# Kernel optimization log

Hardware: AMD Instinct MI355X
Metric: run time of the kernel (lower is better)

## Reference

```python
import jax, jax.numpy as jnp
import numpy as np

N = 50000
D_IN = 1024          # BioGPT hidden size
HID = 256            # gnn_hidden_dim
H1, H2 = 4, 1        # heads per layer
NEG_SLOPE = 0.2      # PyG GATv2 default


def _glorot(key, shape):
    fan_in, fan_out = shape[0], shape[-1]
    lim = (6.0 / (fan_in + fan_out)) ** 0.5
    return jax.random.uniform(key, shape, jnp.float32, -lim, lim)


def setup_inputs() -> dict:
    key = jax.random.key(0)
    ks = jax.random.split(key, 12)
    node_features = jax.random.normal(ks[0], (N, D_IN), jnp.float32)
    edge_index = jax.random.randint(ks[1], (2, 400000), 0, N, jnp.int64)
    return {
        "node_features": node_features,
        "edge_index": edge_index,
        # layer 1: GATv2Conv(1024 -> 256, heads=4)
        "W1_l": _glorot(ks[2], (D_IN, H1 * HID)),
        "b1_l": jnp.zeros((H1 * HID,), jnp.float32),
        "W1_r": _glorot(ks[3], (D_IN, H1 * HID)),
        "b1_r": jnp.zeros((H1 * HID,), jnp.float32),
        "att1": _glorot(ks[4], (H1, HID)),
        "bias1": jnp.zeros((H1 * HID,), jnp.float32),
        # layer 2: GATv2Conv(1024 -> 256, heads=1)
        "W2_l": _glorot(ks[5], (H1 * HID, H2 * HID)),
        "b2_l": jnp.zeros((H2 * HID,), jnp.float32),
        "W2_r": _glorot(ks[6], (H1 * HID, H2 * HID)),
        "b2_r": jnp.zeros((H2 * HID,), jnp.float32),
        "att2": _glorot(ks[7], (H2, HID)),
        "bias2": jnp.zeros((H2 * HID,), jnp.float32),
    }


def _gatv2(x, src, dst, Wl, bl, Wr, br, att, bias, heads):
    n = x.shape[0]
    xl = (x @ Wl + bl).reshape(n, heads, HID)  # source-side transform
    xr = (x @ Wr + br).reshape(n, heads, HID)  # target-side transform
    msg = xl[src] + xr[dst]                    # [E, H, C]
    e = jnp.where(msg > 0, msg, NEG_SLOPE * msg)
    alpha = jnp.einsum('ehc,hc->eh', e, att)   # attention logits
    amax = jax.ops.segment_max(alpha, dst, num_segments=n)
    ex = jnp.exp(alpha - amax[dst])
    denom = jax.ops.segment_sum(ex, dst, num_segments=n)
    a = ex / (denom[dst] + 1e-16)              # segment softmax per dst node
    out = jax.ops.segment_sum(a[:, :, None] * xl[src], dst, num_segments=n)
    return out.reshape(n, heads * HID) + bias


def reference(node_features, edge_index, W1_l, b1_l, W1_r, b1_r, att1, bias1,
              W2_l, b2_l, W2_r, b2_r, att2, bias2):
    n = node_features.shape[0]
    loops = jnp.arange(n, dtype=edge_index.dtype)
    src = jnp.concatenate([edge_index[0], loops])  # add self-loops (PyG default)
    dst = jnp.concatenate([edge_index[1], loops])
    x = _gatv2(node_features, src, dst, W1_l, b1_l, W1_r, b1_r, att1, bias1, H1)
    x = jax.nn.relu(x)
    # dropout(p=0.1) is identity in eval mode
    x = _gatv2(x, src, dst, W2_l, b2_l, W2_r, b2_r, att2, bias2, H2)
    return jax.nn.relu(x)
```

## Files before the change

kernel.cpp:

```cpp
#include <hip/hip_runtime.h>
#include <stdint.h>

#define D_IN 1024
#define C1   1024
#define C2   256
#define NEG  0.2f

typedef unsigned int u32;
typedef uint16_t u16;
typedef __attribute__((ext_vector_type(8))) short bf16x8;
typedef __attribute__((ext_vector_type(4))) float f32x4;

__device__ __forceinline__ float bf2f(u32 lo16) { return __uint_as_float(lo16 << 16); }
__device__ __forceinline__ u16 f2bf(float f) {
  u32 u = __float_as_uint(f);
  u += 0x7fffu + ((u >> 16) & 1u);
  return (u16)(u >> 16);
}

__device__ __forceinline__ void gload16(const u16* g, u16* l) {
  __builtin_amdgcn_global_load_lds(
      (const __attribute__((address_space(1))) unsigned int*)g,
      (__attribute__((address_space(3))) unsigned int*)l,
      16, 0, 0);
}

__global__ void cast_x_k(const float* __restrict__ x, u16* __restrict__ A,
                         int nrows, int Mp) {
  long long idx = (long long)blockIdx.x * blockDim.x + threadIdx.x;
  long long total = (long long)Mp * (D_IN / 8);
  if (idx >= total) return;
  long long base = idx * 8;
  int row = (int)(base >> 10);
  u32 o0 = 0, o1 = 0, o2 = 0, o3 = 0;
  if (row < nrows) {
    const float4* px = (const float4*)(x + base);
    float4 v0 = px[0], v1 = px[1];
    o0 = (u32)f2bf(v0.x) | ((u32)f2bf(v0.y) << 16);
    o1 = (u32)f2bf(v0.z) | ((u32)f2bf(v0.w) << 16);
    o2 = (u32)f2bf(v1.x) | ((u32)f2bf(v1.y) << 16);
    o3 = (u32)f2bf(v1.z) | ((u32)f2bf(v1.w) << 16);
  }
  *(uint4*)(A + base) = make_uint4(o0, o1, o2, o3);
}

__global__ void transpose_cast_k(const float* __restrict__ W, u16* __restrict__ Wt,
                                 int K, int Nc) {
  __shared__ float sh[32][33];
  int k0 = blockIdx.x * 32, n0 = blockIdx.y * 32;
  int tx = threadIdx.x, ty = threadIdx.y;
#pragma unroll
  for (int i = 0; i < 32; i += 8)
    sh[ty + i][tx] = W[(long long)(k0 + ty + i) * Nc + (n0 + tx)];
  __syncthreads();
#pragma unroll
  for (int i = 0; i < 32; i += 8)
    Wt[(long long)(n0 + ty + i) * K + (k0 + tx)] = f2bf(sh[tx][ty + i]);
}

__global__ void concat_bias_k(const float* __restrict__ a, const float* __restrict__ b,
                              float* __restrict__ o, int na, int nb) {
  int i = blockIdx.x * 256 + threadIdx.x;
  if (i < na) o[i] = a[i];
  else if (i < na + nb) o[i] = b[i - na];
}

template <int TN>
__global__ __launch_bounds__(512, 2) void gemm8_k(
    const u16* __restrict__ A, const u16* __restrict__ Bt,
    const float* __restrict__ bias, u16* __restrict__ C, int K) {
  __shared__ u16 As[2][2][8192];
  __shared__ u16 Bs[2][2][8192];
  const int nx = gridDim.x, ny = gridDim.y;
  const int nwg = nx * ny;
  int id = blockIdx.y * nx + blockIdx.x;
  int q = nwg >> 3, r = nwg & 7;
  int xcd = id & 7, loc = id >> 3;
  int sid = (xcd < r ? xcd * (q + 1) : r * (q + 1) + (xcd - r) * q) + loc;
  const int m0 = (sid / ny) * 256;
  const int n0 = (sid % ny) * 256;

  const int tid = threadIdx.x;
  const int lane = tid & 63;
  const int wave = tid >> 6;
  const int wm = wave >> 2;
  const int wn = wave & 3;
  const int bh = wn >> 1;
  const int bql = (wn & 1) * 2048;

  const int srow = tid >> 2;
  const int kq   = tid & 3;
  const int ksw  = (kq ^ ((srow >> 1) & 3)) * 8;

  const int nt = K / 64;

  const u16* gA[2] = { A + (long long)(m0 + srow) * K + ksw,
                       A + (long long)(m0 + 128 + srow) * K + ksw };
  const u16* gB[2] = { Bt + (long long)(n0 + srow) * K + ksw,
                       Bt + (long long)(n0 + 128 + srow) * K + ksw };

  auto stageA = [&](int kt, int h) {
    int db = kt & 1;
    gload16(gA[h] + kt * 64,      &As[db][h][tid * 8]);
    gload16(gA[h] + kt * 64 + 32, &As[db][h][4096 + tid * 8]);
  };
  auto stageB = [&](int kt, int h) {
    int db = kt & 1;
    gload16(gB[h] + kt * 64,      &Bs[db][h][tid * 8]);
    gload16(gB[h] + kt * 64 + 32, &Bs[db][h][4096 + tid * 8]);
  };

  const int rbase = (lane & 15) * 32 + (((lane >> 4) ^ ((lane >> 1) & 3)) << 3);

  f32x4 acc[8][4] = {};
  bf16x8 av[4][2], bv[4][2];

  stageA(0, 0); stageA(0, 1); stageB(0, 0); stageB(0, 1);
  if (nt > 1) {
    stageB(1, 0); stageB(1, 1);
    asm volatile("s_waitcnt vmcnt(4)" ::: "memory");
  } else {
    asm volatile("s_waitcnt vmcnt(0)" ::: "memory");
  }
  __builtin_amdgcn_s_barrier();

  for (int t = 0; t < nt; ++t) {
    const int cur = t & 1;
    const u16* Al = &As[cur][wm][0];
    const u16* Bl = &Bs[cur][bh][0];

    if (t + 1 < nt) stageA(t + 1, 0);
#pragma unroll
    for (int i = 0; i < 4; ++i) {
      av[i][0] = *(const bf16x8*)(Al + i * 512 + rbase);
      av[i][1] = *(const bf16x8*)(Al + 4096 + i * 512 + rbase);
    }
#pragma unroll
    for (int j = 0; j < 2; ++j) {
      bv[j][0] = *(const bf16x8*)(Bl + bql + j * 512 + rbase);
      bv[j][1] = *(const bf16x8*)(Bl + 4096 + bql + j * 512 + rbase);
    }
    __builtin_amdgcn_s_barrier();
    __builtin_amdgcn_s_setprio(1);
#pragma unroll
    for (int i = 0; i < 4; ++i)
#pragma unroll
      for (int j = 0; j < 2; ++j) {
        acc[i][j] = __builtin_amdgcn_mfma_f32_16x16x32_bf16(av[i][0], bv[j][0], acc[i][j], 0, 0, 0);
        acc[i][j] = __builtin_amdgcn_mfma_f32_16x16x32_bf16(av[i][1], bv[j][1], acc[i][j], 0, 0, 0);
      }
    __builtin_amdgcn_s_setprio(0);
    __builtin_amdgcn_s_barrier();

    if (t + 1 < nt) stageA(t + 1, 1);
#pragma unroll
    for (int j = 2; j < 4; ++j) {
      bv[j][0] = *(const bf16x8*)(Bl + bql + j * 512 + rbase);
      bv[j][1] = *(const bf16x8*)(Bl + 4096 + bql + j * 512 + rbase);
    }
    __builtin_amdgcn_s_barrier();
    __builtin_amdgcn_s_setprio(1);
#pragma unroll
    for (int i = 0; i < 4; ++i)
#pragma unroll
      for (int j = 2; j < 4; ++j) {
        acc[i][j] = __builtin_amdgcn_mfma_f32_16x16x32_bf16(av[i][0], bv[j][0], acc[i][j], 0, 0, 0);
        acc[i][j] = __builtin_amdgcn_mfma_f32_16x16x32_bf16(av[i][1], bv[j][1], acc[i][j], 0, 0, 0);
      }
    __builtin_amdgcn_s_setprio(0);
    __builtin_amdgcn_s_barrier();

    if (t + 2 < nt) stageB(t + 2, 0);
#pragma unroll
    for (int i = 0; i < 4; ++i) {
      av[i][0] = *(const bf16x8*)(Al + (4 + i) * 512 + rbase);
      av[i][1] = *(const bf16x8*)(Al + 4096 + (4 + i) * 512 + rbase);
    }
    __builtin_amdgcn_s_barrier();
    __builtin_amdgcn_s_setprio(1);
#pragma unroll
    for (int i = 0; i < 4; ++i)
#pragma unroll
      for (int j = 2; j < 4; ++j) {
        acc[4 + i][j] = __builtin_amdgcn_mfma_f32_16x16x32_bf16(av[i][0], bv[j][0], acc[4 + i][j], 0, 0, 0);
        acc[4 + i][j] = __builtin_amdgcn_mfma_f32_16x16x32_bf16(av[i][1], bv[j][1], acc[4 + i][j], 0, 0, 0);
      }
    __builtin_amdgcn_s_setprio(0);
    __builtin_amdgcn_s_barrier();

    if (t + 2 < nt) stageB(t + 2, 1);
    __builtin_amdgcn_s_barrier();
    __builtin_amdgcn_s_setprio(1);
#pragma unroll
    for (int i = 0; i < 4; ++i)
#pragma unroll
      for (int j = 0; j < 2; ++j) {
        acc[4 + i][j] = __builtin_amdgcn_mfma_f32_16x16x32_bf16(av[i][0], bv[j][0], acc[4 + i][j], 0, 0, 0);
        acc[4 + i][j] = __builtin_amdgcn_mfma_f32_16x16x32_bf16(av[i][1], bv[j][1], acc[4 + i][j], 0, 0, 0);
      }
    __builtin_amdgcn_s_setprio(0);
    if (t + 2 < nt) {
      asm volatile("s_waitcnt vmcnt(4)" ::: "memory");
    } else if (t + 1 < nt) {
      asm volatile("s_waitcnt vmcnt(0)" ::: "memory");
    }
    __builtin_amdgcn_s_barrier();
  }

#pragma unroll
  for (int mf = 0; mf < 8; ++mf) {
    int r0 = m0 + wm * 128 + mf * 16 + ((lane >> 4) << 2);
#pragma unroll
    for (int nf = 0; nf < 4; ++nf) {
      int c = n0 + wn * 64 + nf * 16 + (lane & 15);
      float b = bias[c];
#pragma unroll
      for (int j = 0; j < 4; ++j)
        C[(long long)(r0 + j) * TN + c] = f2bf(acc[mf][nf][j] + b);
    }
  }
}

__global__ void count_k(const int* __restrict__ ei, int* __restrict__ counts,
                        int E0, int E) {
  for (int e = blockIdx.x * blockDim.x + threadIdx.x; e < E;
       e += gridDim.x * blockDim.x) {
    int dst = (e < E0) ? ei[E0 + e] : e - E0;
    atomicAdd(&counts[dst], 1);
  }
}

__global__ void blocksum_k(const int* __restrict__ counts, int* __restrict__ bsum, int n) {
  int i = blockIdx.x * 256 + threadIdx.x;
  int v = (i < n) ? counts[i] : 0;
#pragma unroll
  for (int off = 1; off < 64; off <<= 1) v += __shfl_xor(v, off);
  __shared__ int sh[4];
  if ((threadIdx.x & 63) == 0) sh[threadIdx.x >> 6] = v;
  __syncthreads();
  if (threadIdx.x == 0) bsum[blockIdx.x] = sh[0] + sh[1] + sh[2] + sh[3];
}

__global__ void scanb_k(const int* __restrict__ bsum, int* __restrict__ boff,
                        int nb, int* __restrict__ indptr, int n, int E) {
  __shared__ int sh[256];
  int i = threadIdx.x;
  int v = (i < nb) ? bsum[i] : 0;
  sh[i] = v;
  __syncthreads();
  int sum = v;
  for (int off = 1; off < 256; off <<= 1) {
    int t = (i >= off) ? sh[i - off] : 0;
    __syncthreads();
    sum += t;
    sh[i] = sum;
    __syncthreads();
  }
  if (i < nb) boff[i] = sum - v;
  if (i == 0) indptr[n] = E;
}

__global__ void scanf_k(const int* __restrict__ counts, const int* __restrict__ boff,
                        int* __restrict__ indptr, int n) {
  __shared__ int sh[256];
  int b = blockIdx.x;
  int i = b * 256 + threadIdx.x;
  int v = (i < n) ? counts[i] : 0;
  sh[threadIdx.x] = v;
  __syncthreads();
  int sum = v;
  for (int off = 1; off < 256; off <<= 1) {
    int t = (threadIdx.x >= off) ? sh[threadIdx.x - off] : 0;
    __syncthreads();
    sum += t;
    sh[threadIdx.x] = sum;
    __syncthreads();
  }
  if (i < n) indptr[i] = boff[b] + sum - v;
}

__global__ void scatter_k(const int* __restrict__ ei, const int* __restrict__ indptr,
                          int* __restrict__ cursor, int* __restrict__ esrc,
                          int E0, int E) {
  for (int e = blockIdx.x * blockDim.x + threadIdx.x; e < E;
       e += gridDim.x * blockDim.x) {
    int dst, src;
    if (e < E0) { src = ei[e]; dst = ei[E0 + e]; } else { src = dst = e - E0; }
    int pos = atomicAdd(&cursor[dst], 1);
    esrc[indptr[dst] + pos] = src;
  }
}

__global__ __launch_bounds__(256) void fused_edge1_k(
    const u16* __restrict__ XLR, const int* __restrict__ indptr,
    const int* __restrict__ esrc, const float* __restrict__ att,
    const float* __restrict__ bias, u16* __restrict__ X2, int N) {
  int d = blockIdx.x;
  int tid = threadIdx.x;
  int c0 = tid * 4;
  if (d >= N) {
    *(ushort4*)(X2 + (long long)d * C1 + c0) = make_ushort4(0, 0, 0, 0);
    return;
  }
  ushort4 xr4 = *(const ushort4*)(XLR + (long long)d * 2048 + 1024 + c0);
  float xr0 = bf2f(xr4.x), xr1 = bf2f(xr4.y), xr2 = bf2f(xr4.z), xr3 = bf2f(xr4.w);
  float4 at = *(const float4*)(att + c0);

  float m = -INFINITY, l = 0.f;
  float a0 = 0.f, a1 = 0.f, a2 = 0.f, a3 = 0.f;
  int p = indptr[d], pend = indptr[d + 1];
  ushort4 z4 = make_ushort4(0, 0, 0, 0);
#define LD1(ix) (*(const ushort4*)(XLR + (long long)esrc[ix] * 2048 + c0))
  ushort4 qa = (p < pend) ? LD1(p) : z4;
  ushort4 qb = (p + 1 < pend) ? LD1(p + 1) : z4;
  ushort4 ra = (p + 2 < pend) ? LD1(p + 2) : z4;
  ushort4 rb = (p + 3 < pend) ? LD1(p + 3) : z4;
  int i = p;
  for (; i + 1 < pend; i += 2) {
    ushort4 ca = qa, cb = qb;
    qa = ra; qb = rb;
    ra = (i + 4 < pend) ? LD1(i + 4) : z4;
    rb = (i + 5 < pend) ? LD1(i + 5) : z4;
    float xa0 = bf2f(ca.x), xa1 = bf2f(ca.y), xa2 = bf2f(ca.z), xa3 = bf2f(ca.w);
    float xb0 = bf2f(cb.x), xb1 = bf2f(cb.y), xb2 = bf2f(cb.z), xb3 = bf2f(cb.w);
    float ta0 = xa0 + xr0, ta1 = xa1 + xr1, ta2 = xa2 + xr2, ta3 = xa3 + xr3;
    float tb0 = xb0 + xr0, tb1 = xb1 + xr1, tb2 = xb2 + xr2, tb3 = xb3 + xr3;
    ta0 = ta0 > 0.f ? ta0 : NEG * ta0;  ta1 = ta1 > 0.f ? ta1 : NEG * ta1;
    ta2 = ta2 > 0.f ? ta2 : NEG * ta2;  ta3 = ta3 > 0.f ? ta3 : NEG * ta3;
    tb0 = tb0 > 0.f ? tb0 : NEG * tb0;  tb1 = tb1 > 0.f ? tb1 : NEG * tb1;
    tb2 = tb2 > 0.f ? tb2 : NEG * tb2;  tb3 = tb3 > 0.f ? tb3 : NEG * tb3;
    float sa = at.x * ta0 + at.y * ta1 + at.z * ta2 + at.w * ta3;
    float sb = at.x * tb0 + at.y * tb1 + at.z * tb2 + at.w * tb3;
#pragma unroll
    for (int off = 1; off < 64; off <<= 1) {
      sa += __shfl_xor(sa, off);
      sb += __shfl_xor(sb, off);
    }
    float mnew = fmaxf(fmaxf(m, sa), sb);
    float scale = __expf(m - mnew);
    float wa = __expf(sa - mnew);
    float wb = __expf(sb - mnew);
    l = l * scale + wa + wb;
    a0 = a0 * scale + wa * xa0 + wb * xb0;
    a1 = a1 * scale + wa * xa1 + wb * xb1;
    a2 = a2 * scale + wa * xa2 + wb * xb2;
    a3 = a3 * scale + wa * xa3 + wb * xb3;
    m = mnew;
  }
  if (i < pend) {
    float xa0 = bf2f(qa.x), xa1 = bf2f(qa.y), xa2 = bf2f(qa.z), xa3 = bf2f(qa.w);
    float ta0 = xa0 + xr0, ta1 = xa1 + xr1, ta2 = xa2 + xr2, ta3 = xa3 + xr3;
    ta0 = ta0 > 0.f ? ta0 : NEG * ta0;  ta1 = ta1 > 0.f ? ta1 : NEG * ta1;
    ta2 = ta2 > 0.f ? ta2 : NEG * ta2;  ta3 = ta3 > 0.f ? ta3 : NEG * ta3;
    float sa = at.x * ta0 + at.y * ta1 + at.z * ta2 + at.w * ta3;
#pragma unroll
    for (int off = 1; off < 64; off <<= 1) sa += __shfl_xor(sa, off);
    float mnew = fmaxf(m, sa);
    float scale = __expf(m - mnew);
    float wa = __expf(sa - mnew);
    l = l * scale + wa;
    a0 = a0 * scale + wa * xa0;
    a1 = a1 * scale + wa * xa1;
    a2 = a2 * scale + wa * xa2;
    a3 = a3 * scale + wa * xa3;
  }
#undef LD1
  float inv = 1.f / (l + 1e-16f);
  float4 b = *(const float4*)(bias + c0);
  ushort4 o;
  o.x = f2bf(fmaxf(a0 * inv + b.x, 0.f));
  o.y = f2bf(fmaxf(a1 * inv + b.y, 0.f));
  o.z = f2bf(fmaxf(a2 * inv + b.z, 0.f));
  o.w = f2bf(fmaxf(a3 * inv + b.w, 0.f));
  *(ushort4*)(X2 + (long long)d * C1 + c0) = o;
}

__global__ __launch_bounds__(256) void fused_edge2_k(
    const u16* __restrict__ XLR, const int* __restrict__ indptr,
    const int* __restrict__ esrc, const float* __restrict__ att,
    const float* __restrict__ bias, float* __restrict__ out, int N) {
  int d = blockIdx.x * 4 + (threadIdx.x >> 6);
  if (d >= N) return;
  int lane = threadIdx.x & 63;
  int c0 = lane * 4;
  ushort4 xr4 = *(const ushort4*)(XLR + (long long)d * 512 + 256 + c0);
  float xr0 = bf2f(xr4.x), xr1 = bf2f(xr4.y), xr2 = bf2f(xr4.z), xr3 = bf2f(xr4.w);
  float4 at = *(const float4*)(att + c0);

  float m = -INFINITY, l = 0.f;
  float a0 = 0.f, a1 = 0.f, a2 = 0.f, a3 = 0.f;
  int p = indptr[d], pend = indptr[d + 1];
  ushort4 z4 = make_ushort4(0, 0, 0, 0);
#define LD2(ix) (*(const ushort4*)(XLR + (long long)esrc[ix] * 512 + c0))
  ushort4 qa = (p < pend) ? LD2(p) : z4;
  ushort4 qb = (p + 1 < pend) ? LD2(p + 1) : z4;
  ushort4 ra = (p + 2 < pend) ? LD2(p + 2) : z4;
  ushort4 rb = (p + 3 < pend) ? LD2(p + 3) : z4;
  int i = p;
  for (; i + 1 < pend; i += 2) {
    ushort4 ca = qa, cb = qb;
    qa = ra; qb = rb;
    ra = (i + 4 < pend) ? LD2(i + 4) : z4;
    rb = (i + 5 < pend) ? LD2(i + 5) : z4;
    float xa0 = bf2f(ca.x), xa1 = bf2f(ca.y), xa2 = bf2f(ca.z), xa3 = bf2f(ca.w);
    float xb0 = bf2f(cb.x), xb1 = bf2f(cb.y), xb2 = bf2f(cb.z), xb3 = bf2f(cb.w);
    float ta0 = xa0 + xr0, ta1 = xa1 + xr1, ta2 = xa2 + xr2, ta3 = xa3 + xr3;
    float tb0 = xb0 + xr0, tb1 = xb1 + xr1, tb2 = xb2 + xr2, tb3 = xb3 + xr3;
    ta0 = ta0 > 0.f ? ta0 : NEG * ta0;  ta1 = ta1 > 0.f ? ta1 : NEG * ta1;
    ta2 = ta2 > 0.f ? ta2 : NEG * ta2;  ta3 = ta3 > 0.f ? ta3 : NEG * ta3;
    tb0 = tb0 > 0.f ? tb0 : NEG * tb0;  tb1 = tb1 > 0.f ? tb1 : NEG * tb1;
    tb2 = tb2 > 0.f ? tb2 : NEG * tb2;  tb3 = tb3 > 0.f ? tb3 : NEG * tb3;
    float sa = at.x * ta0 + at.y * ta1 + at.z * ta2 + at.w * ta3;
    float sb = at.x * tb0 + at.y * tb1 + at.z * tb2 + at.w * tb3;
#pragma unroll
    for (int off = 1; off < 64; off <<= 1) {
      sa += __shfl_xor(sa, off);
      sb += __shfl_xor(sb, off);
    }
    float mnew = fmaxf(fmaxf(m, sa), sb);
    float scale = __expf(m - mnew);
    float wa = __expf(sa - mnew);
    float wb = __expf(sb - mnew);
    l = l * scale + wa + wb;
    a0 = a0 * scale + wa * xa0 + wb * xb0;
    a1 = a1 * scale + wa * xa1 + wb * xb1;
    a2 = a2 * scale + wa * xa2 + wb * xb2;
    a3 = a3 * scale + wa * xa3 + wb * xb3;
    m = mnew;
  }
  if (i < pend) {
    float xa0 = bf2f(qa.x), xa1 = bf2f(qa.y), xa2 = bf2f(qa.z), xa3 = bf2f(qa.w);
    float ta0 = xa0 + xr0, ta1 = xa1 + xr1, ta2 = xa2 + xr2, ta3 = xa3 + xr3;
    ta0 = ta0 > 0.f ? ta0 : NEG * ta0;  ta1 = ta1 > 0.f ? ta1 : NEG * ta1;
    ta2 = ta2 > 0.f ? ta2 : NEG * ta2;  ta3 = ta3 > 0.f ? ta3 : NEG * ta3;
    float sa = at.x * ta0 + at.y * ta1 + at.z * ta2 + at.w * ta3;
#pragma unroll
    for (int off = 1; off < 64; off <<= 1) sa += __shfl_xor(sa, off);
    float mnew = fmaxf(m, sa);
    float scale = __expf(m - mnew);
    float wa = __expf(sa - mnew);
    l = l * scale + wa;
    a0 = a0 * scale + wa * xa0;
    a1 = a1 * scale + wa * xa1;
    a2 = a2 * scale + wa * xa2;
    a3 = a3 * scale + wa * xa3;
  }
#undef LD2
  float inv = 1.f / (l + 1e-16f);
  float4 b = *(const float4*)(bias + c0);
  float4 o;
  o.x = fmaxf(a0 * inv + b.x, 0.f);
  o.y = fmaxf(a1 * inv + b.y, 0.f);
  o.z = fmaxf(a2 * inv + b.z, 0.f);
  o.w = fmaxf(a3 * inv + b.w, 0.f);
  *(float4*)(out + (long long)d * C2 + c0) = o;
}

extern "C" void kernel_launch(void* const* d_in, const int* in_sizes, int n_in,
                              void* d_out, int out_size, void* d_ws, size_t ws_size,
                              hipStream_t stream) {
  const float* x     = (const float*)d_in[0];
  const int*   ei    = (const int*)d_in[1];
  const float* W1l   = (const float*)d_in[2];
  const float* b1l   = (const float*)d_in[3];
  const float* W1r   = (const float*)d_in[4];
  const float* b1r   = (const float*)d_in[5];
  const float* att1  = (const float*)d_in[6];
  const float* bias1 = (const float*)d_in[7];
  const float* W2l   = (const float*)d_in[8];
  const float* b2l   = (const float*)d_in[9];
  const float* W2r   = (const float*)d_in[10];
  const float* b2r   = (const float*)d_in[11];
  const float* att2  = (const float*)d_in[12];
  const float* bias2 = (const float*)d_in[13];

  const int N  = in_sizes[0] / D_IN;
  const int E0 = in_sizes[1] / 2;
  const int E  = E0 + N;
  const int Mp = (N + 255) & ~255;
  const int NB = (N + 255) / 256;

  char* p = (char*)d_ws;
  auto alloc = [&](size_t bytes) -> char* {
    char* r = p;
    p += (bytes + 255) & ~(size_t)255;
    return r;
  };
  u16* A_bf  = (u16*)alloc((size_t)Mp * D_IN * 2);
  u16* XLR1  = (u16*)alloc((size_t)Mp * 2048 * 2);
  u16* W1t   = (u16*)alloc((size_t)2048 * D_IN * 2);
  u16* W2t   = (u16*)alloc((size_t)512 * C1 * 2);
  float* bc1 = (float*)alloc(2048 * 4);
  float* bc2 = (float*)alloc(512 * 4);
  int* counts = (int*)alloc((size_t)N * 4);
  int* cursor = (int*)alloc((size_t)N * 4);
  int* indptr = (int*)alloc((size_t)(N + 1) * 4);
  int* esrc   = (int*)alloc((size_t)E * 4);
  int* bsum   = (int*)alloc((size_t)NB * 4);
  int* boff   = (int*)alloc((size_t)NB * 4);
  u16* X2   = A_bf;
  u16* XLR2 = XLR1;

  size_t need = (size_t)(p - (char*)d_ws);
  if (ws_size < need) {
    hipMemsetAsync(d_out, 0xFF, 4, stream);
    return;
  }

  hipMemsetAsync(counts, 0, (size_t)N * 4, stream);
  hipMemsetAsync(cursor, 0, (size_t)N * 4, stream);

  {
    long long tot = (long long)Mp * (D_IN / 8);
    cast_x_k<<<(int)((tot + 255) / 256), 256, 0, stream>>>(x, A_bf, N, Mp);
  }
  dim3 tb(32, 8);
  transpose_cast_k<<<dim3(D_IN / 32, C1 / 32), tb, 0, stream>>>(W1l, W1t, D_IN, C1);
  transpose_cast_k<<<dim3(D_IN / 32, C1 / 32), tb, 0, stream>>>(W1r, W1t + (size_t)1024 * D_IN, D_IN, C1);
  transpose_cast_k<<<dim3(C1 / 32, C2 / 32), tb, 0, stream>>>(W2l, W2t, C1, C2);
  transpose_cast_k<<<dim3(C1 / 32, C2 / 32), tb, 0, stream>>>(W2r, W2t + (size_t)256 * C1, C1, C2);
  concat_bias_k<<<8, 256, 0, stream>>>(b1l, b1r, bc1, 1024, 1024);
  concat_bias_k<<<2, 256, 0, stream>>>(b2l, b2r, bc2, 256, 256);

  count_k<<<1024, 256, 0, stream>>>(ei, counts, E0, E);
  blocksum_k<<<NB, 256, 0, stream>>>(counts, bsum, N);
  scanb_k<<<1, 256, 0, stream>>>(bsum, boff, NB, indptr, N, E);
  scanf_k<<<NB, 256, 0, stream>>>(counts, boff, indptr, N);
  scatter_k<<<1024, 256, 0, stream>>>(ei, indptr, cursor, esrc, E0, E);

  gemm8_k<2048><<<dim3(Mp / 256, 2048 / 256), 512, 0, stream>>>(A_bf, W1t, bc1, XLR1, D_IN);
  fused_edge1_k<<<Mp, 256, 0, stream>>>(XLR1, indptr, esrc, att1, bias1, X2, N);

  gemm8_k<512><<<dim3(Mp / 256, 512 / 256), 512, 0, stream>>>(X2, W2t, bc2, XLR2, C1);
  fused_edge2_k<<<(N + 3) / 4, 256, 0, stream>>>(XLR2, indptr, esrc, att2, bias2,
                                                 (float*)d_out, N);
}
```

Before: 783.0 us.

## Fuse fp32-to-bf16 input cast into first GEMM's A-tile loading

Removes the separate cast_x_k pass. The layer-1 GEMM now reads fp32 node features directly into registers, converts them with v_cvt_pk_bf16_f32 and writes them to LDS, with out-of-range rows clamped to the last row. This saves writing and re-reading a bf16 copy of the 50000x1024 input. The bf16 GEMM path also reorders its A/B staging so A is prefetched earlier with different vmcnt waits. The trade-off is that the fp32 A path uses register-staged loads plus extra LDS waits instead of async direct-to-LDS loads, which may lower GEMM efficiency.

```diff
diff --git a/kernel.cpp b/kernel.cpp
--- a/kernel.cpp
+++ b/kernel.cpp
@@ -17,6 +17,11 @@
   u += 0x7fffu + ((u >> 16) & 1u);
   return (u16)(u >> 16);
 }
+__device__ __forceinline__ u32 cvtpk_bf16(float lo, float hi) {
+  u32 d;
+  asm("v_cvt_pk_bf16_f32 %0, %1, %2" : "=v"(d) : "v"(lo), "v"(hi));
+  return d;
+}
 
 __device__ __forceinline__ void gload16(const u16* g, u16* l) {
   __builtin_amdgcn_global_load_lds(
@@ -25,25 +30,6 @@
       16, 0, 0);
 }
 
-__global__ void cast_x_k(const float* __restrict__ x, u16* __restrict__ A,
-                         int nrows, int Mp) {
-  long long idx = (long long)blockIdx.x * blockDim.x + threadIdx.x;
-  long long total = (long long)Mp * (D_IN / 8);
-  if (idx >= total) return;
-  long long base = idx * 8;
-  int row = (int)(base >> 10);
-  u32 o0 = 0, o1 = 0, o2 = 0, o3 = 0;
-  if (row < nrows) {
-    const float4* px = (const float4*)(x + base);
-    float4 v0 = px[0], v1 = px[1];
-    o0 = (u32)f2bf(v0.x) | ((u32)f2bf(v0.y) << 16);
-    o1 = (u32)f2bf(v0.z) | ((u32)f2bf(v0.w) << 16);
-    o2 = (u32)f2bf(v1.x) | ((u32)f2bf(v1.y) << 16);
-    o3 = (u32)f2bf(v1.z) | ((u32)f2bf(v1.w) << 16);
-  }
-  *(uint4*)(A + base) = make_uint4(o0, o1, o2, o3);
-}
-
 __global__ void transpose_cast_k(const float* __restrict__ W, u16* __restrict__ Wt,
                                  int K, int Nc) {
   __shared__ float sh[32][33];
@@ -65,10 +51,12 @@
   else if (i < na + nb) o[i] = b[i - na];
 }
 
-template <int TN>
+template <int TN, bool F32A>
 __global__ __launch_bounds__(512, 2) void gemm8_k(
-    const u16* __restrict__ A, const u16* __restrict__ Bt,
-    const float* __restrict__ bias, u16* __restrict__ C, int K) {
+    const void* __restrict__ Ap, const u16* __restrict__ Bt,
+    const float* __restrict__ bias, u16* __restrict__ C, int K, int NR) {
+  const u16*   Ab = (const u16*)Ap;
+  const float* Af = (const float*)Ap;
   __shared__ u16 As[2][2][8192];
   __shared__ u16 Bs[2][2][8192];
   const int nx = gridDim.x, ny = gridDim.y;
@@ -94,15 +82,26 @@
 
   const int nt = K / 64;
 
-  const u16* gA[2] = { A + (long long)(m0 + srow) * K + ksw,
-                       A + (long long)(m0 + 128 + srow) * K + ksw };
+  const u16* gA[2];
+  const float* gAf[2];
+  if constexpr (F32A) {
+    int r0 = m0 + srow;       if (r0 >= NR) r0 = NR - 1;
+    int r1 = m0 + 128 + srow; if (r1 >= NR) r1 = NR - 1;
+    gAf[0] = Af + (long long)r0 * K + ksw;
+    gAf[1] = Af + (long long)r1 * K + ksw;
+  } else {
+    gA[0] = Ab + (long long)(m0 + srow) * K + ksw;
+    gA[1] = Ab + (long long)(m0 + 128 + srow) * K + ksw;
+  }
   const u16* gB[2] = { Bt + (long long)(n0 + srow) * K + ksw,
                        Bt + (long long)(n0 + 128 + srow) * K + ksw };
 
   auto stageA = [&](int kt, int h) {
-    int db = kt & 1;
-    gload16(gA[h] + kt * 64,      &As[db][h][tid * 8]);
-    gload16(gA[h] + kt * 64 + 32, &As[db][h][4096 + tid * 8]);
+    if constexpr (!F32A) {
+      int db = kt & 1;
+      gload16(gA[h] + kt * 64,      &As[db][h][tid * 8]);
+      gload16(gA[h] + kt * 64 + 32, &As[db][h][4096 + tid * 8]);
+    }
   };
   auto stageB = [&](int kt, int h) {
     int db = kt & 1;
@@ -110,17 +109,55 @@
     gload16(gB[h] + kt * 64 + 32, &Bs[db][h][4096 + tid * 8]);
   };
 
+  float4 afv[4];
+  auto loadAf = [&](int kt, int h) {
+    if constexpr (F32A) {
+      const float* s = gAf[h] + kt * 64;
+      afv[0] = *(const float4*)(s);
+      afv[1] = *(const float4*)(s + 4);
+      afv[2] = *(const float4*)(s + 32);
+      afv[3] = *(const float4*)(s + 36);
+    }
+  };
+  auto writeAf = [&](int kt, int h) {
+    if constexpr (F32A) {
+      int db = kt & 1;
+      uint4 w0, w1;
+      w0.x = cvtpk_bf16(afv[0].x, afv[0].y); w0.y = cvtpk_bf16(afv[0].z, afv[0].w);
+      w0.z = cvtpk_bf16(afv[1].x, afv[1].y); w0.w = cvtpk_bf16(afv[1].z, afv[1].w);
+      w1.x = cvtpk_bf16(afv[2].x, afv[2].y); w1.y = cvtpk_bf16(afv[2].z, afv[2].w);
+      w1.z = cvtpk_bf16(afv[3].x, afv[3].y); w1.w = cvtpk_bf16(afv[3].z, afv[3].w);
+      *(uint4*)(&As[db][h][tid * 8]) = w0;
+      *(uint4*)(&As[db][h][4096 + tid * 8]) = w1;
+    }
+  };
+
   const int rbase = (lane & 15) * 32 + (((lane >> 4) ^ ((lane >> 1) & 3)) << 3);
 
   f32x4 acc[8][4] = {};
   bf16x8 av[4][2], bv[4][2];
 
-  stageA(0, 0); stageA(0, 1); stageB(0, 0); stageB(0, 1);
-  if (nt > 1) {
-    stageB(1, 0); stageB(1, 1);
-    asm volatile("s_waitcnt vmcnt(4)" ::: "memory");
+  if constexpr (F32A) {
+    loadAf(0, 0);
+    stageB(0, 0); stageB(0, 1);
+    writeAf(0, 0);
+    loadAf(0, 1);
+    if (nt > 1) { stageB(1, 0); stageB(1, 1); }
+    writeAf(0, 1);
+    asm volatile("s_waitcnt lgkmcnt(0)" ::: "memory");
+    if (nt > 1) {
+      asm volatile("s_waitcnt vmcnt(4)" ::: "memory");
+    } else {
+      asm volatile("s_waitcnt vmcnt(0)" ::: "memory");
+    }
   } else {
-    asm volatile("s_waitcnt vmcnt(0)" ::: "memory");
+    stageA(0, 0); stageA(0, 1); stageB(0, 0); stageB(0, 1);
+    if (nt > 1) {
+      stageA(1, 0);
+      asm volatile("s_waitcnt vmcnt(2)" ::: "memory");
+    } else {
+      asm volatile("s_waitcnt vmcnt(0)" ::: "memory");
+    }
   }
   __builtin_amdgcn_s_barrier();
 
@@ -129,7 +166,7 @@
     const u16* Al = &As[cur][wm][0];
     const u16* Bl = &Bs[cur][bh][0];
 
-    if (t + 1 < nt) stageA(t + 1, 0);
+    if (F32A && t + 1 < nt) loadAf(t + 1, 0);
 #pragma unroll
     for (int i = 0; i < 4; ++i) {
       av[i][0] = *(const bf16x8*)(Al + i * 512 + rbase);
@@ -140,6 +177,7 @@
       bv[j][0] = *(const bf16x8*)(Bl + bql + j * 512 + rbase);
       bv[j][1] = *(const bf16x8*)(Bl + 4096 + bql + j * 512 + rbase);
     }
+    if (!F32A && t + 1 < nt) stageA(t + 1, 1);
     __builtin_amdgcn_s_barrier();
     __builtin_amdgcn_s_setprio(1);
 #pragma unroll
@@ -150,14 +188,19 @@
         acc[i][j] = __builtin_amdgcn_mfma_f32_16x16x32_bf16(av[i][1], bv[j][1], acc[i][j], 0, 0, 0);
       }
     __builtin_amdgcn_s_setprio(0);
-    __builtin_amdgcn_s_barrier();
-
-    if (t + 1 < nt) stageA(t + 1, 1);
+    if (F32A && t + 1 < nt) {
+      writeAf(t + 1, 0);
+      asm volatile("s_waitcnt lgkmcnt(0)" ::: "memory");
+    }
+    __builtin_amdgcn_s_barrier();
+
+    if (F32A && t + 1 < nt) loadAf(t + 1, 1);
 #pragma unroll
     for (int j = 2; j < 4; ++j) {
       bv[j][0] = *(const bf16x8*)(Bl + bql + j * 512 + rbase);
       bv[j][1] = *(const bf16x8*)(Bl + 4096 + bql + j * 512 + rbase);
     }
+    if (!F32A && t + 1 < nt) stageB(t + 1, 0);
     __builtin_amdgcn_s_barrier();
     __builtin_amdgcn_s_setprio(1);
 #pragma unroll
@@ -168,14 +211,19 @@
         acc[i][j] = __builtin_amdgcn_mfma_f32_16x16x32_bf16(av[i][1], bv[j][1], acc[i][j], 0, 0, 0);
       }
     __builtin_amdgcn_s_setprio(0);
-    __builtin_amdgcn_s_barrier();
-
-    if (t + 2 < nt) stageB(t + 2, 0);
+    if (F32A && t + 1 < nt) {
+      writeAf(t + 1, 1);
+      asm volatile("s_waitcnt lgkmcnt(0)" ::: "memory");
+    }
+    __builtin_amdgcn_s_barrier();
+
+    if (F32A && t + 2 < nt) stageB(t + 2, 0);
 #pragma unroll
     for (int i = 0; i < 4; ++i) {
       av[i][0] = *(const bf16x8*)(Al + (4 + i) * 512 + rbase);
       av[i][1] = *(const bf16x8*)(Al + 4096 + (4 + i) * 512 + rbase);
     }
+    if (!F32A && t + 1 < nt) stageB(t + 1, 1);
     __builtin_amdgcn_s_barrier();
     __builtin_amdgcn_s_setprio(1);
 #pragma unroll
@@ -188,7 +236,11 @@
     __builtin_amdgcn_s_setprio(0);
     __builtin_amdgcn_s_barrier();
 
-    if (t + 2 < nt) stageB(t + 2, 1);
+    if (F32A) {
+      if (t + 2 < nt) stageB(t + 2, 1);
+    } else {
+      if (t + 2 < nt) stageA(t + 2, 0);
+    }
     __builtin_amdgcn_s_barrier();
     __builtin_amdgcn_s_setprio(1);
 #pragma unroll
@@ -200,7 +252,11 @@
       }
     __builtin_amdgcn_s_setprio(0);
     if (t + 2 < nt) {
-      asm volatile("s_waitcnt vmcnt(4)" ::: "memory");
+      if (F32A) {
+        asm volatile("s_waitcnt vmcnt(4)" ::: "memory");
+      } else {
+        asm volatile("s_waitcnt vmcnt(2)" ::: "memory");
+      }
     } else if (t + 1 < nt) {
       asm volatile("s_waitcnt vmcnt(0)" ::: "memory");
     }
@@ -486,7 +542,7 @@
     p += (bytes + 255) & ~(size_t)255;
     return r;
   };
-  u16* A_bf  = (u16*)alloc((size_t)Mp * D_IN * 2);
+  u16* X2    = (u16*)alloc((size_t)Mp * D_IN * 2);
   u16* XLR1  = (u16*)alloc((size_t)Mp * 2048 * 2);
   u16* W1t   = (u16*)alloc((size_t)2048 * D_IN * 2);
   u16* W2t   = (u16*)alloc((size_t)512 * C1 * 2);
@@ -498,7 +554,6 @@
   int* esrc   = (int*)alloc((size_t)E * 4);
   int* bsum   = (int*)alloc((size_t)NB * 4);
   int* boff   = (int*)alloc((size_t)NB * 4);
-  u16* X2   = A_bf;
   u16* XLR2 = XLR1;
 
   size_t need = (size_t)(p - (char*)d_ws);
@@ -510,10 +565,6 @@
   hipMemsetAsync(counts, 0, (size_t)N * 4, stream);
   hipMemsetAsync(cursor, 0, (size_t)N * 4, stream);
 
-  {
-    long long tot = (long long)Mp * (D_IN / 8);
-    cast_x_k<<<(int)((tot + 255) / 256), 256, 0, stream>>>(x, A_bf, N, Mp);
-  }
   dim3 tb(32, 8);
   transpose_cast_k<<<dim3(D_IN / 32, C1 / 32), tb, 0, stream>>>(W1l, W1t, D_IN, C1);
   transpose_cast_k<<<dim3(D_IN / 32, C1 / 32), tb, 0, stream>>>(W1r, W1t + (size_t)1024 * D_IN, D_IN, C1);
@@ -528,10 +579,12 @@
   scanf_k<<<NB, 256, 0, stream>>>(counts, boff, indptr, N);
   scatter_k<<<1024, 256, 0, stream>>>(ei, indptr, cursor, esrc, E0, E);
 
-  gemm8_k<2048><<<dim3(Mp / 256, 2048 / 256), 512, 0, stream>>>(A_bf, W1t, bc1, XLR1, D_IN);
+  gemm8_k<2048, true><<<dim3(Mp / 256, 2048 / 256), 512, 0, stream>>>(
+      x, W1t, bc1, XLR1, D_IN, N);
   fused_edge1_k<<<Mp, 256, 0, stream>>>(XLR1, indptr, esrc, att1, bias1, X2, N);
 
-  gemm8_k<512><<<dim3(Mp / 256, 512 / 256), 512, 0, stream>>>(X2, W2t, bc2, XLR2, C1);
+  gemm8_k<512, false><<<dim3(Mp / 256, 512 / 256), 512, 0, stream>>>(
+      X2, W2t, bc2, XLR2, C1, N);
   fused_edge2_k<<<(N + 3) / 4, 256, 0, stream>>>(XLR2, indptr, esrc, att2, bias2,
                                                  (float*)d_out, N);
 }
```

After: 789.8 us. No clear change (+0.9%).

## Shorten GEMM prefetch distance and merge weight, bias and memset prep launches

Applied to the files above, without the earlier changes.

The GEMM main loop now prefetches tile t+1 for both A and B in four half-tile stages spread across the compute phases, plus the first A half of t+2, instead of prefetching B two tiles ahead. The waitcnt thresholds drop from 4 to 2 to match. The four weight transpose-casts are merged into one 3D-grid launch, the two bias concatenations into one launch, and the two memsets into a single contiguous memset. The goal is fewer small launches and a different overlap between global-to-LDS loads and MFMA work, at the cost of a shorter prefetch lead for B and a memset that relies on counts and cursor being adjacent in the workspace.

```diff
diff --git a/kernel.cpp b/kernel.cpp
--- a/kernel.cpp
+++ b/kernel.cpp
@@ -44,10 +44,21 @@
   *(uint4*)(A + base) = make_uint4(o0, o1, o2, o3);
 }
 
-__global__ void transpose_cast_k(const float* __restrict__ W, u16* __restrict__ Wt,
-                                 int K, int Nc) {
+__global__ void prep_w_k(const float* __restrict__ W1l, const float* __restrict__ W1r,
+                         const float* __restrict__ W2l, const float* __restrict__ W2r,
+                         u16* __restrict__ W1t, u16* __restrict__ W2t) {
   __shared__ float sh[32][33];
-  int k0 = blockIdx.x * 32, n0 = blockIdx.y * 32;
+  int z = blockIdx.z;
+  const float* W;
+  u16* Wt;
+  int K = 1024, Nc;
+  if (z == 0)      { W = W1l; Wt = W1t;                         Nc = 1024; }
+  else if (z == 1) { W = W1r; Wt = W1t + (size_t)1024 * 1024;   Nc = 1024; }
+  else if (z == 2) { W = W2l; Wt = W2t;                         Nc = 256;  }
+  else             { W = W2r; Wt = W2t + (size_t)256 * 1024;    Nc = 256;  }
+  int n0 = blockIdx.y * 32;
+  if (n0 >= Nc) return;
+  int k0 = blockIdx.x * 32;
   int tx = threadIdx.x, ty = threadIdx.y;
 #pragma unroll
   for (int i = 0; i < 32; i += 8)
@@ -58,11 +69,14 @@
     Wt[(long long)(n0 + ty + i) * K + (k0 + tx)] = f2bf(sh[tx][ty + i]);
 }
 
-__global__ void concat_bias_k(const float* __restrict__ a, const float* __restrict__ b,
-                              float* __restrict__ o, int na, int nb) {
+__global__ void prep_b_k(const float* __restrict__ b1l, const float* __restrict__ b1r,
+                         const float* __restrict__ b2l, const float* __restrict__ b2r,
+                         float* __restrict__ bc1, float* __restrict__ bc2) {
   int i = blockIdx.x * 256 + threadIdx.x;
-  if (i < na) o[i] = a[i];
-  else if (i < na + nb) o[i] = b[i - na];
+  if (i < 1024) bc1[i] = b1l[i];
+  else if (i < 2048) bc1[i] = b1r[i - 1024];
+  else if (i < 2304) bc2[i - 2048] = b2l[i - 2048];
+  else if (i < 2560) bc2[i - 2048] = b2r[i - 2304];
 }
 
 template <int TN>
@@ -117,8 +131,8 @@
 
   stageA(0, 0); stageA(0, 1); stageB(0, 0); stageB(0, 1);
   if (nt > 1) {
-    stageB(1, 0); stageB(1, 1);
-    asm volatile("s_waitcnt vmcnt(4)" ::: "memory");
+    stageA(1, 0);
+    asm volatile("s_waitcnt vmcnt(2)" ::: "memory");
   } else {
     asm volatile("s_waitcnt vmcnt(0)" ::: "memory");
   }
@@ -129,7 +143,6 @@
     const u16* Al = &As[cur][wm][0];
     const u16* Bl = &Bs[cur][bh][0];
 
-    if (t + 1 < nt) stageA(t + 1, 0);
 #pragma unroll
     for (int i = 0; i < 4; ++i) {
       av[i][0] = *(const bf16x8*)(Al + i * 512 + rbase);
@@ -140,6 +153,7 @@
       bv[j][0] = *(const bf16x8*)(Bl + bql + j * 512 + rbase);
       bv[j][1] = *(const bf16x8*)(Bl + 4096 + bql + j * 512 + rbase);
     }
+    if (t + 1 < nt) stageA(t + 1, 1);
     __builtin_amdgcn_s_barrier();
     __builtin_amdgcn_s_setprio(1);
 #pragma unroll
@@ -152,12 +166,12 @@
     __builtin_amdgcn_s_setprio(0);
     __builtin_amdgcn_s_barrier();
 
-    if (t + 1 < nt) stageA(t + 1, 1);
 #pragma unroll
     for (int j = 2; j < 4; ++j) {
       bv[j][0] = *(const bf16x8*)(Bl + bql + j * 512 + rbase);
       bv[j][1] = *(const bf16x8*)(Bl + 4096 + bql + j * 512 + rbase);
     }
+    if (t + 1 < nt) stageB(t + 1, 0);
     __builtin_amdgcn_s_barrier();
     __builtin_amdgcn_s_setprio(1);
 #pragma unroll
@@ -170,12 +184,12 @@
     __builtin_amdgcn_s_setprio(0);
     __builtin_amdgcn_s_barrier();
 
-    if (t + 2 < nt) stageB(t + 2, 0);
 #pragma unroll
     for (int i = 0; i < 4; ++i) {
       av[i][0] = *(const bf16x8*)(Al + (4 + i) * 512 + rbase);
       av[i][1] = *(const bf16x8*)(Al + 4096 + (4 + i) * 512 + rbase);
     }
+    if (t + 1 < nt) stageB(t + 1, 1);
     __builtin_amdgcn_s_barrier();
     __builtin_amdgcn_s_setprio(1);
 #pragma unroll
@@ -188,7 +202,7 @@
     __builtin_amdgcn_s_setprio(0);
     __builtin_amdgcn_s_barrier();
 
-    if (t + 2 < nt) stageB(t + 2, 1);
+    if (t + 2 < nt) stageA(t + 2, 0);
     __builtin_amdgcn_s_barrier();
     __builtin_amdgcn_s_setprio(1);
 #pragma unroll
@@ -200,7 +214,7 @@
       }
     __builtin_amdgcn_s_setprio(0);
     if (t + 2 < nt) {
-      asm volatile("s_waitcnt vmcnt(4)" ::: "memory");
+      asm volatile("s_waitcnt vmcnt(2)" ::: "memory");
     } else if (t + 1 < nt) {
       asm volatile("s_waitcnt vmcnt(0)" ::: "memory");
     }
@@ -507,20 +521,15 @@
     return;
   }
 
-  hipMemsetAsync(counts, 0, (size_t)N * 4, stream);
-  hipMemsetAsync(cursor, 0, (size_t)N * 4, stream);
+  hipMemsetAsync(counts, 0, (size_t)((char*)cursor - (char*)counts) + (size_t)N * 4,
+                 stream);
 
   {
     long long tot = (long long)Mp * (D_IN / 8);
     cast_x_k<<<(int)((tot + 255) / 256), 256, 0, stream>>>(x, A_bf, N, Mp);
   }
-  dim3 tb(32, 8);
-  transpose_cast_k<<<dim3(D_IN / 32, C1 / 32), tb, 0, stream>>>(W1l, W1t, D_IN, C1);
-  transpose_cast_k<<<dim3(D_IN / 32, C1 / 32), tb, 0, stream>>>(W1r, W1t + (size_t)1024 * D_IN, D_IN, C1);
-  transpose_cast_k<<<dim3(C1 / 32, C2 / 32), tb, 0, stream>>>(W2l, W2t, C1, C2);
-  transpose_cast_k<<<dim3(C1 / 32, C2 / 32), tb, 0, stream>>>(W2r, W2t + (size_t)256 * C1, C1, C2);
-  concat_bias_k<<<8, 256, 0, stream>>>(b1l, b1r, bc1, 1024, 1024);
-  concat_bias_k<<<2, 256, 0, stream>>>(b2l, b2r, bc2, 256, 256);
+  prep_w_k<<<dim3(32, 32, 4), dim3(32, 8), 0, stream>>>(W1l, W1r, W2l, W2r, W1t, W2t);
+  prep_b_k<<<10, 256, 0, stream>>>(b1l, b1r, b2l, b2r, bc1, bc2);
 
   count_k<<<1024, 256, 0, stream>>>(ei, counts, E0, E);
   blocksum_k<<<NB, 256, 0, stream>>>(counts, bsum, N);
```

Result: faster. 686.1 us (-12.4%).
